# Performance work log

Measured on AMD Instinct MI355X. Metric: run time of the kernel, lower is better.

## Reference

```python
import jax, jax.numpy as jnp
import numpy as np

N = 16384          # num nodes (adj is dense NxN)
INPUT_DIM = 512
HIDDEN = 128
E_POS = 524288
E_NEG = 524288


def setup_inputs() -> dict:
    key = jax.random.key(0)
    k1, k2, k3, k4, k5, k6, k7 = jax.random.split(key, 7)
    X = jax.random.normal(k1, (N, INPUT_DIM), dtype=jnp.float32)
    adj = jax.random.uniform(k2, (N, N), dtype=jnp.float32)
    train_edges = jax.random.randint(k3, (E_POS, 2), 0, N, dtype=jnp.int64)
    train_false_edges = jax.random.randint(k4, (E_NEG, 2), 0, N, dtype=jnp.int64)
    # parameters (xavier / kaiming scale approximated with uniform bounds)
    b1 = float(np.sqrt(6.0 / (INPUT_DIM + HIDDEN)))
    weight = jax.random.uniform(k5, (INPUT_DIM, HIDDEN), minval=-b1, maxval=b1, dtype=jnp.float32)
    b2 = float(np.sqrt(6.0 / (2 * HIDDEN + HIDDEN)))
    weight_two = jax.random.uniform(k6, (2 * HIDDEN, HIDDEN), minval=-b2, maxval=b2, dtype=jnp.float32)
    b3 = float(np.sqrt(6.0 / HIDDEN) / np.sqrt(2.0))  # kaiming_uniform a=1
    weight_three = jax.random.uniform(k7, (HIDDEN, 1), minval=-b3, maxval=b3, dtype=jnp.float32)
    return {"X": X, "adj": adj, "weight": weight, "weight_two": weight_two,
            "weight_three": weight_three, "train_edges": train_edges,
            "train_false_edges": train_false_edges}


def reference(X, adj, weight, weight_two, weight_three, train_edges, train_false_edges):
    # encode: Z = adj @ (X @ W)
    Z = adj @ (X @ weight)                                  # [N, H]
    edges = jnp.concatenate([train_edges, train_false_edges], axis=0)  # [E, 2]
    # decode: vectorized gather-concat replacing the per-edge Python loop
    z_pair = jnp.concatenate([Z[edges[:, 0]], Z[edges[:, 1]]], axis=1)  # [E, 2H]
    h = jax.nn.relu(z_pair) @ weight_two @ weight_three      # [E, 1]
    return jax.nn.sigmoid(h)
```

## Files before the change

kernel.cpp:

```cpp
#include <hip/hip_runtime.h>


#define N_NODES 16384
#define IN_DIM  512
#define HID     128
#define E_POS_N 524288
#define E_TOT   1048576

typedef __bf16 bf16x8 __attribute__((ext_vector_type(8)));
typedef float  f32x4  __attribute__((ext_vector_type(4)));
typedef unsigned short us8 __attribute__((ext_vector_type(8)));
typedef unsigned short us4 __attribute__((ext_vector_type(4)));

__device__ __forceinline__ bf16x8 ldsb(const void* p){
  return __builtin_bit_cast(bf16x8, *reinterpret_cast<const us8*>(p));
}
__device__ __forceinline__ void gload16(const void* g, void* l){
  __builtin_amdgcn_global_load_lds(
      (const __attribute__((address_space(1))) unsigned int*)g,
      (__attribute__((address_space(3))) unsigned int*)l, 16, 0, 0);
}

__device__ __forceinline__ void split8(const float* f, bf16x8& hi, bf16x8& lo){
  unsigned u[8];
#pragma unroll
  for (int i = 0; i < 8; ++i) u[i] = __float_as_uint(f[i]);
  uint4 hv;
  hv.x = __builtin_amdgcn_perm(u[1], u[0], 0x07060302u);
  hv.y = __builtin_amdgcn_perm(u[3], u[2], 0x07060302u);
  hv.z = __builtin_amdgcn_perm(u[5], u[4], 0x07060302u);
  hv.w = __builtin_amdgcn_perm(u[7], u[6], 0x07060302u);
  hi = __builtin_bit_cast(bf16x8, hv);
  bf16x8 lv;
#pragma unroll
  for (int i = 0; i < 8; ++i)
    lv[i] = (__bf16)(f[i] - __uint_as_float(u[i] & 0xFFFF0000u));
  lo = lv;
}

__global__ __launch_bounds__(512) void prep_kernel(const float* __restrict__ W,
                                                   const float* __restrict__ w2,
                                                   const float* __restrict__ w3,
                                                   unsigned short* __restrict__ bfW,
                                                   float* __restrict__ w23){
  const int blk = blockIdx.x, tid = threadIdx.x;
  if (blk < 16){
    const int c = tid & 127, g = tid >> 7;
    float f[8];
#pragma unroll
    for (int j = 0; j < 8; ++j) f[j] = W[(blk * 32 + g * 8 + j) * HID + c];
    bf16x8 hi, lo; split8(f, hi, lo);
    const int sw = (c & 7) << 4;
    char* tb = (char*)bfW + blk * 16384 + c * 128;
    *(us8*)(tb + ((g * 16) ^ sw))      = __builtin_bit_cast(us8, hi);
    *(us8*)(tb + ((64 + g * 16) ^ sw)) = __builtin_bit_cast(us8, lo);
  } else if (tid < 256){
    float acc = 0.f;
#pragma unroll 4
    for (int k = 0; k < HID; ++k) acc = fmaf(w2[tid * HID + k], w3[k], acc);
    w23[tid] = acc;
  }
}

__global__ __launch_bounds__(256) void xw_kernel(const float* __restrict__ X,
                                                 const unsigned short* __restrict__ bfW,
                                                 unsigned short* __restrict__ bfB){
  __shared__ alignas(16) char lds[4][24576];
  const int tid = threadIdx.x, lane = tid & 63, w = tid >> 6;
  const int blk = blockIdx.x;
  const int g = lane >> 4, l15 = lane & 15;

  int aoff[4][2], boffH[2], boffL[2];
#pragma unroll
  for (int m = 0; m < 4; ++m){
    const int r = m * 16 + l15, sw = (r & 7) << 4;
    aoff[m][0] = r * 128 + ((g * 32) ^ sw);
    aoff[m][1] = r * 128 + ((g * 32 + 16) ^ sw);
  }
#pragma unroll
  for (int n = 0; n < 2; ++n){
    const int c = (w & 3) * 32 + n * 16 + l15, sw = (c & 7) << 4;
    boffH[n] = 8192 + c * 128 + ((g * 16) ^ sw);
    boffL[n] = 8192 + c * 128 + ((64 + g * 16) ^ sw);
  }

  const char* xsrc[2];
#pragma unroll
  for (int i = 0; i < 2; ++i){
    const int r = i * 32 + (tid >> 3);
    xsrc[i] = (const char*)X + ((size_t)(blk * 64 + r) * IN_DIM) * 4
            + (((tid & 7) * 16) ^ ((r & 7) << 4));
  }
  const char* bsrc = (const char*)bfW + tid * 16;

#define XSTAGE(buf, tt) do { \
    gload16(xsrc[0] + (tt) * 128, (buf) + tid * 16); \
    gload16(xsrc[1] + (tt) * 128, (buf) + 4096 + tid * 16); \
    gload16(bsrc + (size_t)(tt) * 16384,         (buf) + 8192  + tid * 16); \
    gload16(bsrc + (size_t)(tt) * 16384 + 4096,  (buf) + 12288 + tid * 16); \
    gload16(bsrc + (size_t)(tt) * 16384 + 8192,  (buf) + 16384 + tid * 16); \
    gload16(bsrc + (size_t)(tt) * 16384 + 12288, (buf) + 20480 + tid * 16); \
  } while (0)

  f32x4 acc[4][2] = {};
  auto compute = [&](const char* bp){
    bf16x8 bHv[2], bLv[2];
#pragma unroll
    for (int n = 0; n < 2; ++n){ bHv[n] = ldsb(bp + boffH[n]); bLv[n] = ldsb(bp + boffL[n]); }
#pragma unroll
    for (int m = 0; m < 4; ++m){
      f32x4 v0 = *(const f32x4*)(bp + aoff[m][0]);
      f32x4 v1 = *(const f32x4*)(bp + aoff[m][1]);
      float f[8] = {v0[0], v0[1], v0[2], v0[3], v1[0], v1[1], v1[2], v1[3]};
      bf16x8 aH, aL; split8(f, aH, aL);
      __builtin_amdgcn_s_setprio(1);
#pragma unroll
      for (int n = 0; n < 2; ++n) acc[m][n] = __builtin_amdgcn_mfma_f32_16x16x32_bf16(aH, bHv[n], acc[m][n], 0, 0, 0);
#pragma unroll
      for (int n = 0; n < 2; ++n) acc[m][n] = __builtin_amdgcn_mfma_f32_16x16x32_bf16(aH, bLv[n], acc[m][n], 0, 0, 0);
#pragma unroll
      for (int n = 0; n < 2; ++n) acc[m][n] = __builtin_amdgcn_mfma_f32_16x16x32_bf16(aL, bHv[n], acc[m][n], 0, 0, 0);
      __builtin_amdgcn_s_setprio(0);
    }
  };

  XSTAGE(lds[0], 0); XSTAGE(lds[1], 1); XSTAGE(lds[2], 2);
  asm volatile("s_waitcnt vmcnt(12)" ::: "memory");
  __builtin_amdgcn_s_barrier();

  const int nt = IN_DIM / 32;
#pragma unroll 1
  for (int t = 0; t < nt; ++t){
    char* bp = lds[t & 3];
    if (t + 3 < nt) XSTAGE(lds[(t + 3) & 3], t + 3);
    compute(bp);
    if (t + 3 < nt)      asm volatile("s_waitcnt vmcnt(12)" ::: "memory");
    else if (t + 2 < nt) asm volatile("s_waitcnt vmcnt(6)" ::: "memory");
    else if (t + 1 < nt) asm volatile("s_waitcnt vmcnt(0)" ::: "memory");
    if (t + 1 < nt) __builtin_amdgcn_s_barrier();
  }
#undef XSTAGE

#pragma unroll
  for (int m = 0; m < 4; ++m){
#pragma unroll
    for (int n = 0; n < 2; ++n){
      const int col = (w & 3) * 32 + n * 16 + l15;
      const int T   = 2 * blk + (m >> 1);
      const int g2  = (2 * m + (g >> 1)) & 3;
      const int sw  = (col & 7) << 4;
      char* tb = (char*)bfB + (size_t)T * 16384 + col * 128;
      uint2 hv;
      hv.x = __builtin_amdgcn_perm(__float_as_uint(acc[m][n][1]), __float_as_uint(acc[m][n][0]), 0x07060302u);
      hv.y = __builtin_amdgcn_perm(__float_as_uint(acc[m][n][3]), __float_as_uint(acc[m][n][2]), 0x07060302u);
      us4 lv;
#pragma unroll
      for (int j = 0; j < 4; ++j){
        unsigned u = __float_as_uint(acc[m][n][j]);
        lv[j] = __builtin_bit_cast(unsigned short,
                 (__bf16)(acc[m][n][j] - __uint_as_float(u & 0xFFFF0000u)));
      }
      *(uint2*)(tb + (((g2 * 16) ^ sw) + (g & 1) * 8))      = hv;
      *(uint2*)(tb + (((64 + g2 * 16) ^ sw) + (g & 1) * 8)) = __builtin_bit_cast(uint2, lv);
    }
  }
}

__global__ __launch_bounds__(512, 4) void zgemm_kernel(const float* __restrict__ adj,
                                                       const unsigned short* __restrict__ bfB,
                                                       float* __restrict__ part){
  __shared__ alignas(16) char lds[2][32768];
  const int tid = threadIdx.x, lane = tid & 63, w = tid >> 6;
  const int wm = w >> 1, wn = w & 1;
  const int xcd = blockIdx.x & 7;
  const int s   = xcd & 3;
  const int mt  = ((xcd >> 2) << 6) + (blockIdx.x >> 3);
  const int k0  = s * (N_NODES / 4);
  const int nt  = (N_NODES / 4) / 32;
  const int g = lane >> 4, l15 = lane & 15;

  int aoff[2][2], boffH[4], boffL[4];
#pragma unroll
  for (int m = 0; m < 2; ++m){
    const int r = wm * 32 + m * 16 + l15, sw = (r & 7) << 4;
    aoff[m][0] = r * 128 + ((g * 32) ^ sw);
    aoff[m][1] = r * 128 + ((g * 32 + 16) ^ sw);
  }
#pragma unroll
  for (int n = 0; n < 4; ++n){
    const int c = wn * 64 + n * 16 + l15, sw = (c & 7) << 4;
    boffH[n] = 16384 + c * 128 + ((g * 16) ^ sw);
    boffL[n] = 16384 + c * 128 + ((64 + g * 16) ^ sw);
  }

  const char* asrc[2];
#pragma unroll
  for (int i = 0; i < 2; ++i){
    const int r = i * 64 + (tid >> 3);
    asrc[i] = (const char*)adj + ((size_t)(mt * 128 + r) * N_NODES + k0) * 4
            + (((tid & 7) * 16) ^ ((r & 7) << 4));
  }
  const char* bsrc = (const char*)bfB + (size_t)(k0 >> 5) * 16384 + tid * 16;

#define ZSTAGE(buf, tt) do { \
    gload16(asrc[0] + (size_t)(tt) * 128, (buf) + tid * 16); \
    gload16(asrc[1] + (size_t)(tt) * 128, (buf) + 8192 + tid * 16); \
    gload16(bsrc + (size_t)(tt) * 16384,        (buf) + 16384 + tid * 16); \
    gload16(bsrc + (size_t)(tt) * 16384 + 8192, (buf) + 24576 + tid * 16); \
  } while (0)

  f32x4 acc[2][4] = {};
  auto compute = [&](const char* bp){
    bf16x8 bHv[4], bLv[4];
#pragma unroll
    for (int n = 0; n < 4; ++n){ bHv[n] = ldsb(bp + boffH[n]); bLv[n] = ldsb(bp + boffL[n]); }
#pragma unroll
    for (int m = 0; m < 2; ++m){
      f32x4 v0 = *(const f32x4*)(bp + aoff[m][0]);
      f32x4 v1 = *(const f32x4*)(bp + aoff[m][1]);
      float f[8] = {v0[0], v0[1], v0[2], v0[3], v1[0], v1[1], v1[2], v1[3]};
      bf16x8 aH, aL; split8(f, aH, aL);
      __builtin_amdgcn_s_setprio(1);
#pragma unroll
      for (int n = 0; n < 4; ++n) acc[m][n] = __builtin_amdgcn_mfma_f32_16x16x32_bf16(aH, bHv[n], acc[m][n], 0, 0, 0);
#pragma unroll
      for (int n = 0; n < 4; ++n) acc[m][n] = __builtin_amdgcn_mfma_f32_16x16x32_bf16(aH, bLv[n], acc[m][n], 0, 0, 0);
#pragma unroll
      for (int n = 0; n < 4; ++n) acc[m][n] = __builtin_amdgcn_mfma_f32_16x16x32_bf16(aL, bHv[n], acc[m][n], 0, 0, 0);
      __builtin_amdgcn_s_setprio(0);
    }
  };

  ZSTAGE(lds[0], 0); ZSTAGE(lds[1], 1);
  asm volatile("s_waitcnt vmcnt(4)" ::: "memory");
  __builtin_amdgcn_s_barrier();
  __builtin_amdgcn_sched_barrier(0);

#pragma unroll 1
  for (int t = 0; t < nt; ++t){
    compute(lds[t & 1]);
    __builtin_amdgcn_sched_barrier(0);
    __builtin_amdgcn_s_barrier();
    if (t + 2 < nt) ZSTAGE(lds[t & 1], t + 2);
    if (t + 1 < nt){
      if (t + 2 < nt) asm volatile("s_waitcnt vmcnt(4)" ::: "memory");
      else            asm volatile("s_waitcnt vmcnt(0)" ::: "memory");
      __builtin_amdgcn_s_barrier();
      __builtin_amdgcn_sched_barrier(0);
    }
  }
#undef ZSTAGE

  float* pb = part + (size_t)s * ((size_t)N_NODES * HID);
  const int row0 = mt * 128 + wm * 32;
  const int col0 = wn * 64;
#pragma unroll
  for (int m = 0; m < 2; ++m){
#pragma unroll
    for (int n = 0; n < 4; ++n){
#pragma unroll
      for (int j = 0; j < 4; ++j){
        const int row = row0 + m * 16 + g * 4 + j;
        const int col = col0 + n * 16 + l15;
        pb[(size_t)row * HID + col] = acc[m][n][j];
      }
    }
  }
}

__global__ __launch_bounds__(256) void nodered_kernel(const float* __restrict__ part,
                                                      const float* __restrict__ w23,
                                                      float* __restrict__ aarr,
                                                      float* __restrict__ barr){
  const int lane = threadIdx.x & 63, wv = threadIdx.x >> 6;
  const int n0 = blockIdx.x * 16 + wv * 4;
  const float w1a = w23[lane],       w1b = w23[lane + 64];
  const float w2a = w23[128 + lane], w2b = w23[192 + lane];
  const float* p = part + (size_t)n0 * HID;
  const size_t NH = (size_t)N_NODES * HID;
  float av[4], bv[4];
#pragma unroll
  for (int u = 0; u < 4; ++u){
    float z1 = 0.f, z2 = 0.f;
#pragma unroll
    for (int sI = 0; sI < 4; ++sI){
      z1 += p[sI * NH + u * HID + lane];
      z2 += p[sI * NH + u * HID + lane + 64];
    }
    z1 = fmaxf(z1, 0.f); z2 = fmaxf(z2, 0.f);
    av[u] = z1 * w1a + z2 * w1b;
    bv[u] = z1 * w2a + z2 * w2b;
  }
#pragma unroll
  for (int u = 0; u < 4; ++u){
#pragma unroll
    for (int o = 32; o > 0; o >>= 1){
      av[u] += __shfl_down(av[u], o);
      bv[u] += __shfl_down(bv[u], o);
    }
  }
  if (lane == 0){
#pragma unroll
    for (int u = 0; u < 4; ++u){ aarr[n0 + u] = av[u]; barr[n0 + u] = bv[u]; }
  }
}

__global__ __launch_bounds__(256) void edge_kernel(const int* __restrict__ e0,
                                                   const int* __restrict__ e1,
                                                   const float* __restrict__ aarr,
                                                   const float* __restrict__ barr,
                                                   float* __restrict__ out){
  const int e = (blockIdx.x * 256 + threadIdx.x) * 4;
  const int* ep; int eb;
  if (e < E_POS_N){ ep = e0; eb = e; } else { ep = e1; eb = e - E_POS_N; }
  int4 p0 = *(const int4*)(ep + 2 * eb);
  int4 p1 = *(const int4*)(ep + 2 * eb + 4);
  float4 o;
  o.x = aarr[p0.x] + barr[p0.y];
  o.y = aarr[p0.z] + barr[p0.w];
  o.z = aarr[p1.x] + barr[p1.y];
  o.w = aarr[p1.z] + barr[p1.w];
  o.x = 1.f / (1.f + __expf(-o.x));
  o.y = 1.f / (1.f + __expf(-o.y));
  o.z = 1.f / (1.f + __expf(-o.z));
  o.w = 1.f / (1.f + __expf(-o.w));
  *(float4*)(out + e) = o;
}

extern "C" void kernel_launch(void* const* d_in, const int* in_sizes, int n_in,
                              void* d_out, int out_size, void* d_ws, size_t ws_size,
                              hipStream_t stream){
  const float* X   = (const float*)d_in[0];
  const float* adj = (const float*)d_in[1];
  const float* W   = (const float*)d_in[2];
  const float* W2  = (const float*)d_in[3];
  const float* W3  = (const float*)d_in[4];
  const int*   e0  = (const int*)d_in[5];
  const int*   e1  = (const int*)d_in[6];
  float* out = (float*)d_out;

  char* wsb = (char*)d_ws;
  const size_t MB = 1024 * 1024;
  unsigned short* bfB = (unsigned short*)(wsb);
  unsigned short* bfW = (unsigned short*)(wsb + 8 * MB);
  float* w23  = (float*)(wsb + 8 * MB + 512 * 1024);
  float* aarr = (float*)(wsb + 9 * MB);
  float* barr = (float*)(wsb + 9 * MB + 64 * 1024);
  float* part = (float*)(wsb + 16 * MB);

  hipLaunchKernelGGL(prep_kernel, dim3(17), dim3(512), 0, stream, W, W2, W3, bfW, w23);
  hipLaunchKernelGGL(xw_kernel, dim3(N_NODES / 64), dim3(256), 0, stream, X, bfW, bfB);
  hipLaunchKernelGGL(zgemm_kernel, dim3(512), dim3(512), 0, stream, adj, bfB, part);
  hipLaunchKernelGGL(nodered_kernel, dim3(N_NODES / 16), dim3(256), 0, stream,
                     part, w23, aarr, barr);
  hipLaunchKernelGGL(edge_kernel, dim3(E_TOT / 1024), dim3(256), 0, stream,
                     e0, e1, aarr, barr, out);
}
```

Baseline: 294.7 us.

## Split B operand into hi/lo arrays and load hi fragments directly to registers

The bf16 hi and lo halves of XW now live in separate workspace arrays. In the adjacency GEMM the hi fragments are read straight from global memory into registers, double-buffered one iteration ahead, while only the lo half is staged through LDS. This cuts LDS footprint and LDS read traffic per tile, and the main loop is unrolled by two to alternate register buffers. In exchange each thread issues uncoalesced 16-byte global loads and holds more registers, and the vmcnt waits now also cover the in-flight register loads, which could stall the pipeline.

```diff
diff --git a/kernel.cpp b/kernel.cpp
--- a/kernel.cpp
+++ b/kernel.cpp
@@ -64,7 +64,8 @@
 
 __global__ __launch_bounds__(256) void xw_kernel(const float* __restrict__ X,
                                                  const unsigned short* __restrict__ bfW,
-                                                 unsigned short* __restrict__ bfB){
+                                                 unsigned short* __restrict__ bfHI,
+                                                 unsigned short* __restrict__ bfLO){
   __shared__ alignas(16) char lds[4][24576];
   const int tid = threadIdx.x, lane = tid & 63, w = tid >> 6;
   const int blk = blockIdx.x;
@@ -147,9 +148,7 @@
     for (int n = 0; n < 2; ++n){
       const int col = (w & 3) * 32 + n * 16 + l15;
       const int T   = 2 * blk + (m >> 1);
-      const int g2  = (2 * m + (g >> 1)) & 3;
-      const int sw  = (col & 7) << 4;
-      char* tb = (char*)bfB + (size_t)T * 16384 + col * 128;
+      const int s8  = (2 * m + (g >> 1)) & 3;
       uint2 hv;
       hv.x = __builtin_amdgcn_perm(__float_as_uint(acc[m][n][1]), __float_as_uint(acc[m][n][0]), 0x07060302u);
       hv.y = __builtin_amdgcn_perm(__float_as_uint(acc[m][n][3]), __float_as_uint(acc[m][n][2]), 0x07060302u);
@@ -160,16 +159,20 @@
         lv[j] = __builtin_bit_cast(unsigned short,
                  (__bf16)(acc[m][n][j] - __uint_as_float(u & 0xFFFF0000u)));
       }
-      *(uint2*)(tb + (((g2 * 16) ^ sw) + (g & 1) * 8))      = hv;
-      *(uint2*)(tb + (((64 + g2 * 16) ^ sw) + (g & 1) * 8)) = __builtin_bit_cast(uint2, lv);
+      char* hb = (char*)bfHI + (size_t)T * 8192 + col * 64 + s8 * 16 + (g & 1) * 8;
+      char* lb = (char*)bfLO + (size_t)T * 8192 + (col >> 1) * 128
+               + ((((col & 1) * 64) + s8 * 16) ^ (((col >> 1) & 7) << 4)) + (g & 1) * 8;
+      *(uint2*)hb = hv;
+      *(uint2*)lb = __builtin_bit_cast(uint2, lv);
     }
   }
 }
 
 __global__ __launch_bounds__(512, 4) void zgemm_kernel(const float* __restrict__ adj,
-                                                       const unsigned short* __restrict__ bfB,
+                                                       const unsigned short* __restrict__ bfHI,
+                                                       const unsigned short* __restrict__ bfLO,
                                                        float* __restrict__ part){
-  __shared__ alignas(16) char lds[2][32768];
+  __shared__ alignas(16) char lds[2][24576];
   const int tid = threadIdx.x, lane = tid & 63, w = tid >> 6;
   const int wm = w >> 1, wn = w & 1;
   const int xcd = blockIdx.x & 7;
@@ -179,18 +182,17 @@
   const int nt  = (N_NODES / 4) / 32;
   const int g = lane >> 4, l15 = lane & 15;
 
-  int aoff[2][2], boffH[4], boffL[4];
+  int aoff[2][2], boffL[4];
 #pragma unroll
   for (int m = 0; m < 2; ++m){
     const int r = wm * 32 + m * 16 + l15, sw = (r & 7) << 4;
     aoff[m][0] = r * 128 + ((g * 32) ^ sw);
-    aoff[m][1] = r * 128 + ((g * 32 + 16) ^ sw);
+    aoff[m][1] = aoff[m][0] ^ 16;
   }
 #pragma unroll
   for (int n = 0; n < 4; ++n){
-    const int c = wn * 64 + n * 16 + l15, sw = (c & 7) << 4;
-    boffH[n] = 16384 + c * 128 + ((g * 16) ^ sw);
-    boffL[n] = 16384 + c * 128 + ((64 + g * 16) ^ sw);
+    const int c = wn * 64 + n * 16 + l15;
+    boffL[n] = 16384 + (c >> 1) * 128 + ((((c & 1) * 64) + g * 16) ^ (((c >> 1) & 7) << 4));
   }
 
   const char* asrc[2];
@@ -200,20 +202,34 @@
     asrc[i] = (const char*)adj + ((size_t)(mt * 128 + r) * N_NODES + k0) * 4
             + (((tid & 7) * 16) ^ ((r & 7) << 4));
   }
-  const char* bsrc = (const char*)bfB + (size_t)(k0 >> 5) * 16384 + tid * 16;
+  const char* losrc  = (const char*)bfLO + (size_t)(k0 >> 5) * 8192 + tid * 16;
+  const char* hibase = (const char*)bfHI + (size_t)(k0 >> 5) * 8192
+                     + (wn * 64 + l15) * 64 + g * 16;
 
 #define ZSTAGE(buf, tt) do { \
     gload16(asrc[0] + (size_t)(tt) * 128, (buf) + tid * 16); \
     gload16(asrc[1] + (size_t)(tt) * 128, (buf) + 8192 + tid * 16); \
-    gload16(bsrc + (size_t)(tt) * 16384,        (buf) + 16384 + tid * 16); \
-    gload16(bsrc + (size_t)(tt) * 16384 + 8192, (buf) + 24576 + tid * 16); \
+    gload16(losrc + (size_t)(tt) * 8192,  (buf) + 16384 + tid * 16); \
   } while (0)
 
+#define HILOAD(dst, tt) do { \
+    const char* hp_ = hibase + (size_t)(tt) * 8192; \
+    dst[0] = *(const uint4*)(hp_); \
+    dst[1] = *(const uint4*)(hp_ + 1024); \
+    dst[2] = *(const uint4*)(hp_ + 2048); \
+    dst[3] = *(const uint4*)(hp_ + 3072); \
+  } while (0)
+
   f32x4 acc[2][4] = {};
-  auto compute = [&](const char* bp){
-    bf16x8 bHv[4], bLv[4];
-#pragma unroll
-    for (int n = 0; n < 4; ++n){ bHv[n] = ldsb(bp + boffH[n]); bLv[n] = ldsb(bp + boffL[n]); }
+  uint4 bhA[4], bhB[4];
+
+  auto iter = [&](const uint4* cur, uint4* nxt, int t){
+    HILOAD(nxt, t + 1);
+    __builtin_amdgcn_sched_barrier(0);
+    const char* bp = lds[t & 1];
+    bf16x8 bLv[4];
+#pragma unroll
+    for (int n = 0; n < 4; ++n) bLv[n] = ldsb(bp + boffL[n]);
 #pragma unroll
     for (int m = 0; m < 2; ++m){
       f32x4 v0 = *(const f32x4*)(bp + aoff[m][0]);
@@ -222,34 +238,39 @@
       bf16x8 aH, aL; split8(f, aH, aL);
       __builtin_amdgcn_s_setprio(1);
 #pragma unroll
-      for (int n = 0; n < 4; ++n) acc[m][n] = __builtin_amdgcn_mfma_f32_16x16x32_bf16(aH, bHv[n], acc[m][n], 0, 0, 0);
-#pragma unroll
-      for (int n = 0; n < 4; ++n) acc[m][n] = __builtin_amdgcn_mfma_f32_16x16x32_bf16(aH, bLv[n], acc[m][n], 0, 0, 0);
-#pragma unroll
-      for (int n = 0; n < 4; ++n) acc[m][n] = __builtin_amdgcn_mfma_f32_16x16x32_bf16(aL, bHv[n], acc[m][n], 0, 0, 0);
+      for (int n = 0; n < 4; ++n)
+        acc[m][n] = __builtin_amdgcn_mfma_f32_16x16x32_bf16(aH, __builtin_bit_cast(bf16x8, cur[n]), acc[m][n], 0, 0, 0);
+#pragma unroll
+      for (int n = 0; n < 4; ++n)
+        acc[m][n] = __builtin_amdgcn_mfma_f32_16x16x32_bf16(aH, bLv[n], acc[m][n], 0, 0, 0);
+#pragma unroll
+      for (int n = 0; n < 4; ++n)
+        acc[m][n] = __builtin_amdgcn_mfma_f32_16x16x32_bf16(aL, __builtin_bit_cast(bf16x8, cur[n]), acc[m][n], 0, 0, 0);
       __builtin_amdgcn_s_setprio(0);
     }
-  };
-
-  ZSTAGE(lds[0], 0); ZSTAGE(lds[1], 1);
-  asm volatile("s_waitcnt vmcnt(4)" ::: "memory");
-  __builtin_amdgcn_s_barrier();
-  __builtin_amdgcn_sched_barrier(0);
-
-#pragma unroll 1
-  for (int t = 0; t < nt; ++t){
-    compute(lds[t & 1]);
     __builtin_amdgcn_sched_barrier(0);
     __builtin_amdgcn_s_barrier();
     if (t + 2 < nt) ZSTAGE(lds[t & 1], t + 2);
     if (t + 1 < nt){
-      if (t + 2 < nt) asm volatile("s_waitcnt vmcnt(4)" ::: "memory");
+      if (t + 2 < nt) asm volatile("s_waitcnt vmcnt(3)" ::: "memory");
       else            asm volatile("s_waitcnt vmcnt(0)" ::: "memory");
       __builtin_amdgcn_s_barrier();
       __builtin_amdgcn_sched_barrier(0);
     }
+  };
+
+  ZSTAGE(lds[0], 0); ZSTAGE(lds[1], 1);
+  HILOAD(bhA, 0);
+  asm volatile("s_waitcnt vmcnt(0)" ::: "memory");
+  __builtin_amdgcn_s_barrier();
+
+#pragma unroll 1
+  for (int t = 0; t < nt; t += 2){
+    iter(bhA, bhB, t);
+    iter(bhB, bhA, t + 1);
   }
 #undef ZSTAGE
+#undef HILOAD
 
   float* pb = part + (size_t)s * ((size_t)N_NODES * HID);
   const int row0 = mt * 128 + wm * 32;
@@ -341,16 +362,17 @@
 
   char* wsb = (char*)d_ws;
   const size_t MB = 1024 * 1024;
-  unsigned short* bfB = (unsigned short*)(wsb);
-  unsigned short* bfW = (unsigned short*)(wsb + 8 * MB);
+  unsigned short* bfHI = (unsigned short*)(wsb);
+  unsigned short* bfLO = (unsigned short*)(wsb + 4 * MB);
+  unsigned short* bfW  = (unsigned short*)(wsb + 8 * MB);
   float* w23  = (float*)(wsb + 8 * MB + 512 * 1024);
   float* aarr = (float*)(wsb + 9 * MB);
   float* barr = (float*)(wsb + 9 * MB + 64 * 1024);
   float* part = (float*)(wsb + 16 * MB);
 
   hipLaunchKernelGGL(prep_kernel, dim3(17), dim3(512), 0, stream, W, W2, W3, bfW, w23);
-  hipLaunchKernelGGL(xw_kernel, dim3(N_NODES / 64), dim3(256), 0, stream, X, bfW, bfB);
-  hipLaunchKernelGGL(zgemm_kernel, dim3(512), dim3(512), 0, stream, adj, bfB, part);
+  hipLaunchKernelGGL(xw_kernel, dim3(N_NODES / 64), dim3(256), 0, stream, X, bfW, bfHI, bfLO);
+  hipLaunchKernelGGL(zgemm_kernel, dim3(512), dim3(512), 0, stream, adj, bfHI, bfLO, part);
   hipLaunchKernelGGL(nodered_kernel, dim3(N_NODES / 16), dim3(256), 0, stream,
                      part, w23, aarr, barr);
   hipLaunchKernelGGL(edge_kernel, dim3(E_TOT / 1024), dim3(256), 0, stream,
```

Result: slower. 333.6 us (+13.2%).

## Double K-tile depth in zgemm with split A/B staging and 128KB LDS

Applied to the files above, without the earlier changes.

Restructures the adjacency GEMM main loop to process 64-wide K super-tiles, each computed as two 32-wide sub-steps. A and B are loaded in separate staged groups interleaved between the two sub-steps, with double-buffered 64KB halves of a 128KB LDS allocation. This halves the number of outer iterations and spreads the loads across the iteration to overlap memory with MFMA work. The larger LDS footprint lowers occupancy, with launch bounds reduced from 4 to 2 blocks.

```diff
diff --git a/kernel.cpp b/kernel.cpp
--- a/kernel.cpp
+++ b/kernel.cpp
@@ -166,58 +166,64 @@
   }
 }
 
-__global__ __launch_bounds__(512, 4) void zgemm_kernel(const float* __restrict__ adj,
+__global__ __launch_bounds__(512, 2) void zgemm_kernel(const float* __restrict__ adj,
                                                        const unsigned short* __restrict__ bfB,
                                                        float* __restrict__ part){
-  __shared__ alignas(16) char lds[2][32768];
+  __shared__ alignas(16) char lds[131072];
   const int tid = threadIdx.x, lane = tid & 63, w = tid >> 6;
   const int wm = w >> 1, wn = w & 1;
   const int xcd = blockIdx.x & 7;
   const int s   = xcd & 3;
   const int mt  = ((xcd >> 2) << 6) + (blockIdx.x >> 3);
   const int k0  = s * (N_NODES / 4);
-  const int nt  = (N_NODES / 4) / 32;
+  const int NSUP = (N_NODES / 4) / 64;
   const int g = lane >> 4, l15 = lane & 15;
 
   int aoff[2][2], boffH[4], boffL[4];
 #pragma unroll
   for (int m = 0; m < 2; ++m){
     const int r = wm * 32 + m * 16 + l15, sw = (r & 7) << 4;
-    aoff[m][0] = r * 128 + ((g * 32) ^ sw);
-    aoff[m][1] = r * 128 + ((g * 32 + 16) ^ sw);
+    aoff[m][0] = r * 256 + ((g * 32) ^ sw);
+    aoff[m][1] = r * 256 + ((g * 32 + 16) ^ sw);
   }
 #pragma unroll
   for (int n = 0; n < 4; ++n){
     const int c = wn * 64 + n * 16 + l15, sw = (c & 7) << 4;
-    boffH[n] = 16384 + c * 128 + ((g * 16) ^ sw);
-    boffL[n] = 16384 + c * 128 + ((64 + g * 16) ^ sw);
-  }
-
-  const char* asrc[2];
-#pragma unroll
-  for (int i = 0; i < 2; ++i){
-    const int r = i * 64 + (tid >> 3);
-    asrc[i] = (const char*)adj + ((size_t)(mt * 128 + r) * N_NODES + k0) * 4
-            + (((tid & 7) * 16) ^ ((r & 7) << 4));
-  }
+    boffH[n] = c * 128 + ((g * 16) ^ sw);
+    boffL[n] = c * 128 + ((64 + g * 16) ^ sw);
+  }
+
+  const int arow = tid >> 4;
+  const char* asrc = (const char*)adj
+      + ((size_t)(mt * 128 + arow) * N_NODES + k0) * 4
+      + (((tid & 15) * 16) ^ ((arow & 7) << 4));
+  const size_t ARND = (size_t)32 * N_NODES * 4;
   const char* bsrc = (const char*)bfB + (size_t)(k0 >> 5) * 16384 + tid * 16;
 
-#define ZSTAGE(buf, tt) do { \
-    gload16(asrc[0] + (size_t)(tt) * 128, (buf) + tid * 16); \
-    gload16(asrc[1] + (size_t)(tt) * 128, (buf) + 8192 + tid * 16); \
-    gload16(bsrc + (size_t)(tt) * 16384,        (buf) + 16384 + tid * 16); \
-    gload16(bsrc + (size_t)(tt) * 16384 + 8192, (buf) + 24576 + tid * 16); \
+#define STAGE_A(bo, tt) do { \
+    gload16(asrc + (size_t)(tt) * 256,            lds + (bo) + tid * 16); \
+    gload16(asrc + (size_t)(tt) * 256 + ARND,     lds + (bo) + 8192  + tid * 16); \
+    gload16(asrc + (size_t)(tt) * 256 + 2 * ARND, lds + (bo) + 16384 + tid * 16); \
+    gload16(asrc + (size_t)(tt) * 256 + 3 * ARND, lds + (bo) + 24576 + tid * 16); \
   } while (0)
+#define STAGE_B(bo, tt) do { \
+    gload16(bsrc + (size_t)(2 * (tt)) * 16384,            lds + (bo) + tid * 16); \
+    gload16(bsrc + (size_t)(2 * (tt)) * 16384 + 8192,     lds + (bo) + 8192  + tid * 16); \
+    gload16(bsrc + (size_t)(2 * (tt) + 1) * 16384,        lds + (bo) + 16384 + tid * 16); \
+    gload16(bsrc + (size_t)(2 * (tt) + 1) * 16384 + 8192, lds + (bo) + 24576 + tid * 16); \
+  } while (0)
 
   f32x4 acc[2][4] = {};
-  auto compute = [&](const char* bp){
+  auto compute = [&](int ao, int bo, int sub){
+    const char* bps = lds + bo + sub * 16384;
+    const char* ap  = lds + ao + sub * 128;
     bf16x8 bHv[4], bLv[4];
 #pragma unroll
-    for (int n = 0; n < 4; ++n){ bHv[n] = ldsb(bp + boffH[n]); bLv[n] = ldsb(bp + boffL[n]); }
+    for (int n = 0; n < 4; ++n){ bHv[n] = ldsb(bps + boffH[n]); bLv[n] = ldsb(bps + boffL[n]); }
 #pragma unroll
     for (int m = 0; m < 2; ++m){
-      f32x4 v0 = *(const f32x4*)(bp + aoff[m][0]);
-      f32x4 v1 = *(const f32x4*)(bp + aoff[m][1]);
+      f32x4 v0 = *(const f32x4*)(ap + aoff[m][0]);
+      f32x4 v1 = *(const f32x4*)(ap + aoff[m][1]);
       float f[8] = {v0[0], v0[1], v0[2], v0[3], v1[0], v1[1], v1[2], v1[3]};
       bf16x8 aH, aL; split8(f, aH, aL);
       __builtin_amdgcn_s_setprio(1);
@@ -231,25 +237,31 @@
     }
   };
 
-  ZSTAGE(lds[0], 0); ZSTAGE(lds[1], 1);
-  asm volatile("s_waitcnt vmcnt(4)" ::: "memory");
-  __builtin_amdgcn_s_barrier();
-  __builtin_amdgcn_sched_barrier(0);
+  STAGE_A(0, 0);
+  STAGE_B(65536, 0);
 
 #pragma unroll 1
-  for (int t = 0; t < nt; ++t){
-    compute(lds[t & 1]);
+  for (int t = 0; t < NSUP; ++t){
+    const int ao = (t & 1) ? 32768 : 0;
+    const int bo = 65536 + ((t & 1) ? 32768 : 0);
+    const int an = (t & 1) ? 0 : 32768;
+    const int bn = 65536 + ((t & 1) ? 0 : 32768);
+    asm volatile("s_waitcnt vmcnt(2)" ::: "memory");
+    __builtin_amdgcn_s_barrier();
     __builtin_amdgcn_sched_barrier(0);
+    if (t + 1 < NSUP) STAGE_A(an, t + 1);
+    compute(ao, bo, 0);
+    __builtin_amdgcn_sched_barrier(0);
+    if (t + 1 < NSUP) asm volatile("s_waitcnt vmcnt(4)" ::: "memory");
+    else              asm volatile("s_waitcnt vmcnt(0)" ::: "memory");
     __builtin_amdgcn_s_barrier();
-    if (t + 2 < nt) ZSTAGE(lds[t & 1], t + 2);
-    if (t + 1 < nt){
-      if (t + 2 < nt) asm volatile("s_waitcnt vmcnt(4)" ::: "memory");
-      else            asm volatile("s_waitcnt vmcnt(0)" ::: "memory");
-      __builtin_amdgcn_s_barrier();
-      __builtin_amdgcn_sched_barrier(0);
-    }
-  }
-#undef ZSTAGE
+    __builtin_amdgcn_sched_barrier(0);
+    if (t + 1 < NSUP) STAGE_B(bn, t + 1);
+    compute(ao, bo, 1);
+    __builtin_amdgcn_sched_barrier(0);
+  }
+#undef STAGE_A
+#undef STAGE_B
 
   float* pb = part + (size_t)s * ((size_t)N_NODES * HID);
   const int row0 = mt * 128 + wm * 32;
```

New measurement: 337.2 us. +14.4%, slower.

## Fuse node reduction into Z GEMM, drop split-K, use 64-row tiles with deep pipelining

Applied to the files above, without the earlier changes.

The adj@XW GEMM no longer splits K four ways into a partial buffer. Each block now owns 64 full rows over the whole K range, with a larger LDS ring: a double-buffered 512-wide A tile and a 4-slot B ring. The ReLU and the w23 projection are done in the epilogue through shuffles and a small LDS exchange, which removes the separate node-reduction kernel and the partial-sum write and read traffic. The trade-off is fewer blocks (256 instead of 512), lower occupancy from 128KB of LDS, and more complex wait-count bookkeeping.

```diff
diff --git a/kernel.cpp b/kernel.cpp
--- a/kernel.cpp
+++ b/kernel.cpp
@@ -166,142 +166,146 @@
   }
 }
 
-__global__ __launch_bounds__(512, 4) void zgemm_kernel(const float* __restrict__ adj,
+__global__ __launch_bounds__(512, 2) void zgemm_kernel(const float* __restrict__ adj,
                                                        const unsigned short* __restrict__ bfB,
-                                                       float* __restrict__ part){
-  __shared__ alignas(16) char lds[2][32768];
+                                                       const float* __restrict__ w23,
+                                                       float* __restrict__ aarr,
+                                                       float* __restrict__ barr){
+  __shared__ alignas(16) char lds[131072];
   const int tid = threadIdx.x, lane = tid & 63, w = tid >> 6;
   const int wm = w >> 1, wn = w & 1;
-  const int xcd = blockIdx.x & 7;
-  const int s   = xcd & 3;
-  const int mt  = ((xcd >> 2) << 6) + (blockIdx.x >> 3);
-  const int k0  = s * (N_NODES / 4);
-  const int nt  = (N_NODES / 4) / 32;
+  const int mt = blockIdx.x;
   const int g = lane >> 4, l15 = lane & 15;
 
-  int aoff[2][2], boffH[4], boffL[4];
-#pragma unroll
-  for (int m = 0; m < 2; ++m){
-    const int r = wm * 32 + m * 16 + l15, sw = (r & 7) << 4;
-    aoff[m][0] = r * 128 + ((g * 32) ^ sw);
-    aoff[m][1] = r * 128 + ((g * 32 + 16) ^ sw);
-  }
+  float wa[4], wb[4];
+#pragma unroll
+  for (int n = 0; n < 4; ++n){
+    const int c = wn * 64 + n * 16 + l15;
+    wa[n] = w23[c];
+    wb[n] = w23[128 + c];
+  }
+
+  const int r = wm * 16 + l15;
+  const int swzr = (r & 7) << 4;
+  const int aoff0 = r * 512 + ((g * 32) ^ swzr);
+  const int aoff1 = r * 512 + ((g * 32 + 16) ^ swzr);
+  int boffH[4], boffL[4];
 #pragma unroll
   for (int n = 0; n < 4; ++n){
     const int c = wn * 64 + n * 16 + l15, sw = (c & 7) << 4;
-    boffH[n] = 16384 + c * 128 + ((g * 16) ^ sw);
-    boffL[n] = 16384 + c * 128 + ((64 + g * 16) ^ sw);
-  }
-
-  const char* asrc[2];
-#pragma unroll
-  for (int i = 0; i < 2; ++i){
-    const int r = i * 64 + (tid >> 3);
-    asrc[i] = (const char*)adj + ((size_t)(mt * 128 + r) * N_NODES + k0) * 4
-            + (((tid & 7) * 16) ^ ((r & 7) << 4));
-  }
-  const char* bsrc = (const char*)bfB + (size_t)(k0 >> 5) * 16384 + tid * 16;
-
-#define ZSTAGE(buf, tt) do { \
-    gload16(asrc[0] + (size_t)(tt) * 128, (buf) + tid * 16); \
-    gload16(asrc[1] + (size_t)(tt) * 128, (buf) + 8192 + tid * 16); \
-    gload16(bsrc + (size_t)(tt) * 16384,        (buf) + 16384 + tid * 16); \
-    gload16(bsrc + (size_t)(tt) * 16384 + 8192, (buf) + 24576 + tid * 16); \
+    boffH[n] = c * 128 + ((g * 16) ^ sw);
+    boffL[n] = c * 128 + ((64 + g * 16) ^ sw);
+  }
+
+  const int arw = tid >> 5;
+  const char* asrc = (const char*)adj + ((size_t)(mt * 64 + arw) << 16)
+                   + (((tid & 31) * 16) ^ ((arw & 7) << 4));
+  const char* bsrc = (const char*)bfB + tid * 16;
+
+#define STAGE_AP(abo, tt, p) \
+  gload16(asrc + ((size_t)(p) << 20) + (size_t)(tt) * 512, lds + (abo) + (p) * 8192 + tid * 16)
+#define STAGE_BT(i) do { \
+    const char* bs_ = bsrc + (size_t)(i) * 16384; \
+    char* bd_ = lds + 65536 + ((i) & 3) * 16384 + tid * 16; \
+    gload16(bs_, bd_); gload16(bs_ + 8192, bd_ + 8192); \
   } while (0)
 
-  f32x4 acc[2][4] = {};
-  auto compute = [&](const char* bp){
+  f32x4 acc[4] = {};
+  auto compute = [&](int abo, int s, int bslot){
+    const char* ap = lds + abo + s * 128;
+    const char* bp = lds + 65536 + bslot * 16384;
     bf16x8 bHv[4], bLv[4];
 #pragma unroll
     for (int n = 0; n < 4; ++n){ bHv[n] = ldsb(bp + boffH[n]); bLv[n] = ldsb(bp + boffL[n]); }
-#pragma unroll
-    for (int m = 0; m < 2; ++m){
-      f32x4 v0 = *(const f32x4*)(bp + aoff[m][0]);
-      f32x4 v1 = *(const f32x4*)(bp + aoff[m][1]);
-      float f[8] = {v0[0], v0[1], v0[2], v0[3], v1[0], v1[1], v1[2], v1[3]};
-      bf16x8 aH, aL; split8(f, aH, aL);
-      __builtin_amdgcn_s_setprio(1);
-#pragma unroll
-      for (int n = 0; n < 4; ++n) acc[m][n] = __builtin_amdgcn_mfma_f32_16x16x32_bf16(aH, bHv[n], acc[m][n], 0, 0, 0);
-#pragma unroll
-      for (int n = 0; n < 4; ++n) acc[m][n] = __builtin_amdgcn_mfma_f32_16x16x32_bf16(aH, bLv[n], acc[m][n], 0, 0, 0);
-#pragma unroll
-      for (int n = 0; n < 4; ++n) acc[m][n] = __builtin_amdgcn_mfma_f32_16x16x32_bf16(aL, bHv[n], acc[m][n], 0, 0, 0);
-      __builtin_amdgcn_s_setprio(0);
-    }
+    f32x4 v0 = *(const f32x4*)(ap + aoff0);
+    f32x4 v1 = *(const f32x4*)(ap + aoff1);
+    float f[8] = {v0[0], v0[1], v0[2], v0[3], v1[0], v1[1], v1[2], v1[3]};
+    bf16x8 aH, aL; split8(f, aH, aL);
+    __builtin_amdgcn_s_setprio(1);
+#pragma unroll
+    for (int n = 0; n < 4; ++n) acc[n] = __builtin_amdgcn_mfma_f32_16x16x32_bf16(aH, bHv[n], acc[n], 0, 0, 0);
+#pragma unroll
+    for (int n = 0; n < 4; ++n) acc[n] = __builtin_amdgcn_mfma_f32_16x16x32_bf16(aH, bLv[n], acc[n], 0, 0, 0);
+#pragma unroll
+    for (int n = 0; n < 4; ++n) acc[n] = __builtin_amdgcn_mfma_f32_16x16x32_bf16(aL, bHv[n], acc[n], 0, 0, 0);
+    __builtin_amdgcn_s_setprio(0);
   };
 
-  ZSTAGE(lds[0], 0); ZSTAGE(lds[1], 1);
-  asm volatile("s_waitcnt vmcnt(4)" ::: "memory");
+  STAGE_AP(0, 0, 0); STAGE_AP(0, 0, 1); STAGE_AP(0, 0, 2); STAGE_AP(0, 0, 3);
+  STAGE_BT(0); STAGE_BT(1); STAGE_BT(2);
+  asm volatile("s_waitcnt vmcnt(0)" ::: "memory");
   __builtin_amdgcn_s_barrier();
-  __builtin_amdgcn_sched_barrier(0);
 
 #pragma unroll 1
-  for (int t = 0; t < nt; ++t){
-    compute(lds[t & 1]);
-    __builtin_amdgcn_sched_barrier(0);
-    __builtin_amdgcn_s_barrier();
-    if (t + 2 < nt) ZSTAGE(lds[t & 1], t + 2);
-    if (t + 1 < nt){
-      if (t + 2 < nt) asm volatile("s_waitcnt vmcnt(4)" ::: "memory");
-      else            asm volatile("s_waitcnt vmcnt(0)" ::: "memory");
+  for (int t = 0; t < 128; ++t){
+    const int abo = (t & 1) * 32768;
+    const int abn = ((t + 1) & 1) * 32768;
+    if (t < 127){
+#pragma unroll
+      for (int s = 0; s < 4; ++s){
+        if (s == 0) asm volatile("s_waitcnt vmcnt(2)" ::: "memory");
+        else        asm volatile("s_waitcnt vmcnt(6)" ::: "memory");
+        __builtin_amdgcn_s_barrier();
+        __builtin_amdgcn_sched_barrier(0);
+        STAGE_AP(abn, t + 1, s);
+        STAGE_BT(t * 4 + s + 3);
+        compute(abo, s, (t * 4 + s) & 3);
+        __builtin_amdgcn_sched_barrier(0);
+      }
+    } else {
+      asm volatile("s_waitcnt vmcnt(2)" ::: "memory");
       __builtin_amdgcn_s_barrier();
-      __builtin_amdgcn_sched_barrier(0);
-    }
-  }
-#undef ZSTAGE
-
-  float* pb = part + (size_t)s * ((size_t)N_NODES * HID);
-  const int row0 = mt * 128 + wm * 32;
-  const int col0 = wn * 64;
-#pragma unroll
-  for (int m = 0; m < 2; ++m){
+      STAGE_BT(511);
+      compute(abo, 0, 508 & 3);
+      asm volatile("s_waitcnt vmcnt(5)" ::: "memory");
+      __builtin_amdgcn_s_barrier();
+      compute(abo, 1, 509 & 3);
+      asm volatile("s_waitcnt vmcnt(2)" ::: "memory");
+      __builtin_amdgcn_s_barrier();
+      compute(abo, 2, 510 & 3);
+      asm volatile("s_waitcnt vmcnt(0)" ::: "memory");
+      __builtin_amdgcn_s_barrier();
+      compute(abo, 3, 511 & 3);
+    }
+  }
+#undef STAGE_AP
+#undef STAGE_BT
+
+  float pav[4], pbv[4];
+#pragma unroll
+  for (int j = 0; j < 4; ++j){
+    float pa = 0.f, pb = 0.f;
 #pragma unroll
     for (int n = 0; n < 4; ++n){
-#pragma unroll
-      for (int j = 0; j < 4; ++j){
-        const int row = row0 + m * 16 + g * 4 + j;
-        const int col = col0 + n * 16 + l15;
-        pb[(size_t)row * HID + col] = acc[m][n][j];
-      }
-    }
-  }
-}
-
-__global__ __launch_bounds__(256) void nodered_kernel(const float* __restrict__ part,
-                                                      const float* __restrict__ w23,
-                                                      float* __restrict__ aarr,
-                                                      float* __restrict__ barr){
-  const int lane = threadIdx.x & 63, wv = threadIdx.x >> 6;
-  const int n0 = blockIdx.x * 16 + wv * 4;
-  const float w1a = w23[lane],       w1b = w23[lane + 64];
-  const float w2a = w23[128 + lane], w2b = w23[192 + lane];
-  const float* p = part + (size_t)n0 * HID;
-  const size_t NH = (size_t)N_NODES * HID;
-  float av[4], bv[4];
-#pragma unroll
-  for (int u = 0; u < 4; ++u){
-    float z1 = 0.f, z2 = 0.f;
-#pragma unroll
-    for (int sI = 0; sI < 4; ++sI){
-      z1 += p[sI * NH + u * HID + lane];
-      z2 += p[sI * NH + u * HID + lane + 64];
-    }
-    z1 = fmaxf(z1, 0.f); z2 = fmaxf(z2, 0.f);
-    av[u] = z1 * w1a + z2 * w1b;
-    bv[u] = z1 * w2a + z2 * w2b;
-  }
-#pragma unroll
-  for (int u = 0; u < 4; ++u){
-#pragma unroll
-    for (int o = 32; o > 0; o >>= 1){
-      av[u] += __shfl_down(av[u], o);
-      bv[u] += __shfl_down(bv[u], o);
-    }
-  }
-  if (lane == 0){
-#pragma unroll
-    for (int u = 0; u < 4; ++u){ aarr[n0 + u] = av[u]; barr[n0 + u] = bv[u]; }
+      const float z = fmaxf(acc[n][j], 0.f);
+      pa = fmaf(z, wa[n], pa);
+      pb = fmaf(z, wb[n], pb);
+    }
+#pragma unroll
+    for (int o = 1; o < 16; o <<= 1){
+      pa += __shfl_xor(pa, o);
+      pb += __shfl_xor(pb, o);
+    }
+    pav[j] = pa; pbv[j] = pb;
+  }
+  float* sred = (float*)lds;
+  __syncthreads();
+  if (wn == 1 && l15 == 0){
+#pragma unroll
+    for (int j = 0; j < 4; ++j){
+      const int ri = wm * 16 + g * 4 + j;
+      sred[ri] = pav[j];
+      sred[64 + ri] = pbv[j];
+    }
+  }
+  __syncthreads();
+  if (wn == 0 && l15 == 0){
+#pragma unroll
+    for (int j = 0; j < 4; ++j){
+      const int ri = wm * 16 + g * 4 + j;
+      aarr[mt * 64 + ri] = pav[j] + sred[ri];
+      barr[mt * 64 + ri] = pbv[j] + sred[64 + ri];
+    }
   }
 }
 
@@ -346,13 +350,11 @@
   float* w23  = (float*)(wsb + 8 * MB + 512 * 1024);
   float* aarr = (float*)(wsb + 9 * MB);
   float* barr = (float*)(wsb + 9 * MB + 64 * 1024);
-  float* part = (float*)(wsb + 16 * MB);
 
   hipLaunchKernelGGL(prep_kernel, dim3(17), dim3(512), 0, stream, W, W2, W3, bfW, w23);
   hipLaunchKernelGGL(xw_kernel, dim3(N_NODES / 64), dim3(256), 0, stream, X, bfW, bfB);
-  hipLaunchKernelGGL(zgemm_kernel, dim3(512), dim3(512), 0, stream, adj, bfB, part);
-  hipLaunchKernelGGL(nodered_kernel, dim3(N_NODES / 16), dim3(256), 0, stream,
-                     part, w23, aarr, barr);
+  hipLaunchKernelGGL(zgemm_kernel, dim3(N_NODES / 64), dim3(512), 0, stream,
+                     adj, bfB, w23, aarr, barr);
   hipLaunchKernelGGL(edge_kernel, dim3(E_TOT / 1024), dim3(256), 0, stream,
                      e0, e1, aarr, barr, out);
 }
```

New measurement: 328.5 us. 1.11x slower.
